# Kernel tuning notes

Measured on AMD Instinct MI355X. Metric: run time of the kernel, lower is better.

The kernel has to match this reference:

```python
import jax, jax.numpy as jnp
import numpy as np

K = 3  # kernel size, padding=1, stride=1


def _patches(x):
    # x: [N,C,H,W] -> [N,C,9,H,W] of 3x3 neighborhoods (zero pad 1)
    N, C, H, W = x.shape
    xp = jnp.pad(x, ((0, 0), (0, 0), (1, 1), (1, 1)))
    return jnp.stack([xp[:, :, i:i + H, j:j + W] for i in range(K) for j in range(K)], axis=2)


def _conv25d(x, depth, fx, w0, w1, w2, b):
    # depth-banded 2.5D conv: 3 weight sets selected per (pixel, kernel-tap) by depth band
    N, C, H, W = x.shape
    O = w0.shape[0]
    px = _patches(x)                       # [N,C,9,H,W]
    d = _patches(depth)[:, 0]              # [N,9,H,W]
    center = d[:, K * K // 2:K * K // 2 + 1]  # [N,1,H,W]
    valid = ((d != 0) & (center != 0)).astype(x.dtype)
    d = d * valid
    center = d[:, K * K // 2:K * K // 2 + 1]
    gr = center / fx                       # grid_range, pixel_size = 1
    half = gr * 0.5
    m0 = (jnp.abs(d - (center + gr)) <= half).astype(x.dtype)  # behind plane
    m1 = (jnp.abs(d - center) < half).astype(x.dtype)          # on plane
    m2 = (jnp.abs(d - (center - gr)) <= half).astype(x.dtype)  # in front
    out = jnp.zeros((N, O, H, W), x.dtype)
    for w, m in ((w0, m0), (w1, m1), (w2, m2)):
        out = out + jnp.einsum('ock,nckhw->nohw', w.reshape(O, C, K * K), px * m[:, None])
    return out + b[None, :, None, None]


def _maxpool2(x):
    return jax.lax.reduce_window(x, -jnp.inf, jax.lax.max, (1, 1, 2, 2), (1, 1, 2, 2), 'VALID')


def setup_inputs() -> dict:
    key = jax.random.key(0)
    ks = jax.random.split(key, 16)
    N, H, W = 16, 224, 224

    def xavier(k, shape):
        if len(shape) == 4:
            rf = shape[2] * shape[3]
            fan_in, fan_out = shape[1] * rf, shape[0] * rf
        else:
            fan_out, fan_in = shape
        lim = float(np.sqrt(6.0 / (fan_in + fan_out)))
        return jax.random.uniform(k, shape, jnp.float32, -lim, lim)

    return {
        'x': jax.random.normal(ks[0], (N, 3, H, W), jnp.float32),
        'depth': jax.random.uniform(ks[1], (N, 1, H, W), jnp.float32, 1.0, 5.0),
        'fx': jnp.full((1,), 4.0, jnp.float32),
        'c1_w0': xavier(ks[2], (16, 3, 3, 3)),
        'c1_w1': xavier(ks[3], (16, 3, 3, 3)),
        'c1_w2': xavier(ks[4], (16, 3, 3, 3)),
        'c1_b': jnp.zeros((16,), jnp.float32),
        'c2_w0': xavier(ks[5], (16, 16, 3, 3)),
        'c2_w1': xavier(ks[6], (16, 16, 3, 3)),
        'c2_w2': xavier(ks[7], (16, 16, 3, 3)),
        'c2_b': jnp.zeros((16,), jnp.float32),
        'fc1_w': xavier(ks[8], (128, 16 * (W // 2) * (H // 2))),
        'fc1_b': jnp.zeros((128,), jnp.float32),
        'fc2_w': xavier(ks[9], (10, 128)),
        'fc2_b': jnp.zeros((10,), jnp.float32),
    }


def reference(x, depth, fx, c1_w0, c1_w1, c1_w2, c1_b, c2_w0, c2_w1, c2_w2, c2_b, fc1_w, fc1_b, fc2_w, fc2_b):
    h = jax.nn.relu(_conv25d(x, depth, fx, c1_w0, c1_w1, c1_w2, c1_b))
    h = _maxpool2(jax.nn.relu(_conv25d(h, depth, fx, c2_w0, c2_w1, c2_w2, c2_b)))
    h = h.reshape(h.shape[0], -1)          # [N, 16*112*112]
    h = h @ fc1_w.T + fc1_b                # no relu between fc1/fc2 (matches source)
    h = h @ fc2_w.T + fc2_b
    return jax.nn.log_softmax(h, axis=1)
```

## Files before the change

kernel.cpp:

```cpp
#include <hip/hip_runtime.h>
#include <hip/hip_fp16.h>
#include <stdint.h>

#define HH 224
#define HWD 224
#define HWP (HH*HWD)
#define PH 112
#define PW 112
#define PHW (PH*PW)
#define FCK 200704
#define KSEG 196

typedef _Float16 f16x8 __attribute__((ext_vector_type(8)));
typedef float f32x4 __attribute__((ext_vector_type(4)));

static __device__ __forceinline__ uint32_t pkh2(float a, float b) {
  __half2 h = __floats2half2_rn(a, b);
  return __builtin_bit_cast(uint32_t, h);
}
static __device__ __forceinline__ f32x4 mfma16(uint4 a, uint4 b, f32x4 c) {
  return __builtin_amdgcn_mfma_f32_16x16x32_f16(
      __builtin_bit_cast(f16x8, a), __builtin_bit_cast(f16x8, b), c, 0, 0, 0);
}


__global__ __launch_bounds__(256, 4) void conv1_kernel(
    const float* __restrict__ x, const float* __restrict__ depth,
    const float* __restrict__ fxp,
    const float* __restrict__ w0, const float* __restrict__ w1,
    const float* __restrict__ w2, const float* __restrict__ bias,
    uint32_t* __restrict__ sel, __half* __restrict__ h1t) {
  __shared__ __align__(16) __half ts[324*24];
  __shared__ __align__(16) uint4 wlds[15*64];
  __shared__ float dt[324];
  __shared__ uint32_t sbits[256];
  __shared__ __align__(16) __half hbuf[1024];
  int tid = threadIdx.x;
  int lane = tid & 63, wid = tid >> 6;
  int r = lane & 15;
  int tapPar = lane >> 5;
  int c0 = ((lane >> 4) & 1) * 8;
  float bo = bias[r];
  float fx = fxp[0];

  #pragma unroll
  for (int it = 0; it < 4; ++it) {
    int t = tid + it*256;
    int tc = min(t, 959);
    int ln = tc & 63; int pj = tc >> 6;
    int p = pj / 3, j = pj % 3;
    int o = ln & 15; int tap = p*2 + (ln >> 5);
    int cbase = ((ln >> 4) & 1) * 8;
    const float* wj = (j == 0) ? w0 : (j == 1) ? w1 : w2;
    float f[8];
    #pragma unroll
    for (int e = 0; e < 8; ++e) {
      int c = cbase + e;
      float v = wj[o*27 + min(c,2)*9 + min(tap,8)];
      f[e] = (tap <= 8 && c < 3) ? v : 0.f;
    }
    if (t < 960) {
      uint4 wv = { pkh2(f[0],f[1]), pkh2(f[2],f[3]), pkh2(f[4],f[5]), pkh2(f[6],f[7]) };
      wlds[pj*64 + ln] = wv;
    }
  }

  int tbase = blockIdx.x * 4;
  float pf[2][3]; float pd[2];
  {
    int tile = tbase;
    int n = tile/196, rem = tile%196, br = rem/14, bc = rem%14;
    int y0 = br*16 - 1, x0 = bc*16 - 1;
    const float* xn = x + (size_t)n*3*HWP;
    const float* dn = depth + (size_t)n*HWP;
    #pragma unroll
    for (int it = 0; it < 2; ++it) {
      int p = min(tid + it*256, 323);
      int yy = y0 + p/18, xx = x0 + p%18;
      int gy = min(max(yy,0),HH-1), gx = min(max(xx,0),HWD-1);
      size_t off = (size_t)gy*HWD + gx;
      pf[it][0] = xn[off]; pf[it][1] = xn[HWP+off]; pf[it][2] = xn[2*HWP+off];
      float dv = dn[off];
      pd[it] = (yy>=0 && yy<HH && xx>=0 && xx<HWD) ? dv : 0.f;
    }
  }

  for (int ti = 0; ti < 4; ++ti) {
    int tile = tbase + ti;
    int n = tile/196, rem = tile%196, br = rem/14, bc = rem%14;
    #pragma unroll
    for (int it = 0; it < 2; ++it) {
      int p = tid + it*256;
      if (p < 324) {
        uint4 v0 = { pkh2(pf[it][0], pf[it][1]), pkh2(pf[it][2], 0.f), 0u, 0u };
        uint4 z  = { 0u, 0u, 0u, 0u };
        *(uint4*)(ts + p*24)      = v0;
        *(uint4*)(ts + p*24 + 8)  = z;
        *(uint4*)(ts + p*24 + 16) = z;
        dt[p] = pd[it];
      }
    }
    if (ti < 3) {
      int tile2 = tile + 1;
      int n2 = tile2/196, rem2 = tile2%196, br2 = rem2/14, bc2 = rem2%14;
      int y0 = br2*16 - 1, x0 = bc2*16 - 1;
      const float* xn = x + (size_t)n2*3*HWP;
      const float* dn = depth + (size_t)n2*HWP;
      #pragma unroll
      for (int it = 0; it < 2; ++it) {
        int p = min(tid + it*256, 323);
        int yy = y0 + p/18, xx = x0 + p%18;
        int gy = min(max(yy,0),HH-1), gx = min(max(xx,0),HWD-1);
        size_t off = (size_t)gy*HWD + gx;
        pf[it][0] = xn[off]; pf[it][1] = xn[HWP+off]; pf[it][2] = xn[2*HWP+off];
        float dv = dn[off];
        pd[it] = (yy>=0 && yy<HH && xx>=0 && xx<HWD) ? dv : 0.f;
      }
    }
    __syncthreads();
    {
      int py = tid >> 4, px = tid & 15;
      float c = dt[(py+1)*18 + (px+1)];
      float gr = c / fx;
      float hf = gr * 0.5f;
      uint32_t bits = 0;
      #pragma unroll
      for (int i = 0; i < 3; ++i)
        #pragma unroll
        for (int j = 0; j < 3; ++j) {
          float d = dt[(py+i)*18 + (px+j)];
          int k = i*3 + j;
          uint32_t bb = 0;
          if (fabsf(d - (c + gr)) <= hf) bb |= 1u;
          if (fabsf(d - c) < hf)         bb |= 2u;
          if (fabsf(d - (c - gr)) <= hf) bb |= 4u;
          bits |= bb << (3*k);
        }
      sbits[tid] = bits;
      sel[(size_t)n*HWP + (br*16 + py)*HWD + bc*16 + px] = bits;
    }
    __syncthreads();
    uint32_t svc[4];
    #pragma unroll
    for (int ty = 0; ty < 4; ++ty) svc[ty] = sbits[(wid*4 + ty)*16 + r];
    f32x4 acc[4] = {{0,0,0,0},{0,0,0,0},{0,0,0,0},{0,0,0,0}};
    #pragma unroll
    for (int p = 0; p < 5; ++p) {
      int ta = 2*p, tb = (2*p+1 > 8) ? 8 : 2*p+1;
      int dyL = tapPar ? tb/3 : ta/3;
      int dxL = tapPar ? tb%3 : ta%3;
      int shL = 3*(tapPar ? 2*p+1 : 2*p);
      uint4 a[4];
      #pragma unroll
      for (int ty = 0; ty < 4; ++ty) {
        int ly = wid*4 + ty;
        a[ty] = *(const uint4*)(ts + ((ly + dyL)*18 + (r + dxL))*24 + c0);
      }
      #pragma unroll
      for (int j = 0; j < 3; ++j) {
        uint4 bf = wlds[(p*3 + j)*64 + lane];
        #pragma unroll
        for (int ty = 0; ty < 4; ++ty) {
          uint32_t msk = 0u - ((svc[ty] >> (shL + j)) & 1u);
          uint4 am = { a[ty].x & msk, a[ty].y & msk, a[ty].z & msk, a[ty].w & msk };
          acc[ty] = mfma16(am, bf, acc[ty]);
        }
      }
    }
    #pragma unroll
    for (int ty = 0; ty < 4; ++ty) {
      int gy = br*16 + wid*4 + ty;
      #pragma unroll
      for (int e = 0; e < 4; ++e) {
        float v = fmaxf(acc[ty][e] + bo, 0.f);
        hbuf[wid*256 + ((lane>>4)*4 + e)*16 + r] = __float2half(v);
      }
      uint2 hw = *(uint2*)&hbuf[wid*256 + lane*4];
      *(uint2*)(h1t + ((size_t)(n*HWP + gy*HWD) + bc*16)*16 + lane*4) = hw;
    }
    __syncthreads();
  }
}

__global__ __launch_bounds__(256, 4) void conv2_kernel(
    const __half* __restrict__ h1t, const uint32_t* __restrict__ sel,
    const float* __restrict__ w0, const float* __restrict__ w1,
    const float* __restrict__ w2, const float* __restrict__ bias,
    __half* __restrict__ pooled) {
  __shared__ __align__(16) __half ts[324*24];
  __shared__ __align__(16) uint4 wlds[15*64];
  __shared__ float pl[64*17];
  int tid = threadIdx.x;
  int lane = tid & 63, wid = tid >> 6;
  int r = lane & 15;
  int tapPar = lane >> 5;
  int c0 = ((lane >> 4) & 1) * 8;
  float bo = bias[r];

  #pragma unroll
  for (int it = 0; it < 4; ++it) {
    int t = tid + it*256;
    int tc = min(t, 959);
    int ln = tc & 63; int pj = tc >> 6;
    int p = pj / 3, j = pj % 3;
    int o = ln & 15; int tap = p*2 + (ln >> 5);
    int cbase = ((ln >> 4) & 1) * 8;
    const float* wj = (j == 0) ? w0 : (j == 1) ? w1 : w2;
    const float* wp = wj + o*144 + cbase*9 + tap;
    float f[8];
    #pragma unroll
    for (int e = 0; e < 8; ++e) {
      float v = wp[e*9];
      f[e] = (tap <= 8) ? v : 0.f;
    }
    if (t < 960) {
      uint4 wv = { pkh2(f[0],f[1]), pkh2(f[2],f[3]), pkh2(f[4],f[5]), pkh2(f[6],f[7]) };
      wlds[pj*64 + ln] = wv;
    }
  }

  int tbase = blockIdx.x * 4;
  uint4 st[3]; uint32_t sv[4];
  {
    int tile = tbase;
    int n = tile/196, rem = tile%196, br = rem/14, bc = rem%14;
    int y0 = br*16 - 1, x0 = bc*16 - 1;
    const __half* hn = h1t + (size_t)n*HWP*16;
    #pragma unroll
    for (int it = 0; it < 3; ++it) {
      int w = min(tid + it*256, 647);
      int p = w >> 1, hh = w & 1;
      int gy = min(max(y0 + p/18, 0), HH-1);
      int gx = min(max(x0 + p%18, 0), HWD-1);
      st[it] = *(const uint4*)(hn + ((size_t)(gy*HWD + gx))*16 + hh*8);
    }
    #pragma unroll
    for (int ty = 0; ty < 4; ++ty)
      sv[ty] = sel[(size_t)n*HWP + (br*16 + wid*4 + ty)*HWD + bc*16 + r];
  }

  for (int ti = 0; ti < 4; ++ti) {
    int tile = tbase + ti;
    int n = tile/196, rem = tile%196, br = rem/14, bc = rem%14;
    #pragma unroll
    for (int it = 0; it < 3; ++it) {
      int w = tid + it*256;
      if (w < 648) {
        int p = w >> 1, hh = w & 1;
        *(uint4*)(ts + p*24 + hh*8) = st[it];
      }
    }
    uint32_t svc[4];
    #pragma unroll
    for (int ty = 0; ty < 4; ++ty) svc[ty] = sv[ty];
    if (ti < 3) {
      int tile2 = tile + 1;
      int n2 = tile2/196, rem2 = tile2%196, br2 = rem2/14, bc2 = rem2%14;
      int y0 = br2*16 - 1, x0 = bc2*16 - 1;
      const __half* hn = h1t + (size_t)n2*HWP*16;
      #pragma unroll
      for (int it = 0; it < 3; ++it) {
        int w = min(tid + it*256, 647);
        int p = w >> 1, hh = w & 1;
        int gy = min(max(y0 + p/18, 0), HH-1);
        int gx = min(max(x0 + p%18, 0), HWD-1);
        st[it] = *(const uint4*)(hn + ((size_t)(gy*HWD + gx))*16 + hh*8);
      }
      #pragma unroll
      for (int ty = 0; ty < 4; ++ty)
        sv[ty] = sel[(size_t)n2*HWP + (br2*16 + wid*4 + ty)*HWD + bc2*16 + r];
    }
    __syncthreads();
    f32x4 acc[4] = {{0,0,0,0},{0,0,0,0},{0,0,0,0},{0,0,0,0}};
    #pragma unroll
    for (int p = 0; p < 5; ++p) {
      int ta = 2*p, tb = (2*p+1 > 8) ? 8 : 2*p+1;
      int dyL = tapPar ? tb/3 : ta/3;
      int dxL = tapPar ? tb%3 : ta%3;
      int shL = 3*(tapPar ? 2*p+1 : 2*p);
      uint4 a[4];
      #pragma unroll
      for (int ty = 0; ty < 4; ++ty) {
        int ly = wid*4 + ty;
        a[ty] = *(const uint4*)(ts + ((ly + dyL)*18 + (r + dxL))*24 + c0);
      }
      #pragma unroll
      for (int j = 0; j < 3; ++j) {
        uint4 bf = wlds[(p*3 + j)*64 + lane];
        #pragma unroll
        for (int ty = 0; ty < 4; ++ty) {
          uint32_t msk = 0u - ((svc[ty] >> (shL + j)) & 1u);
          uint4 am = { a[ty].x & msk, a[ty].y & msk, a[ty].z & msk, a[ty].w & msk };
          acc[ty] = mfma16(am, bf, acc[ty]);
        }
      }
    }
    #pragma unroll
    for (int yp = 0; yp < 2; ++yp) {
      f32x4 v0 = acc[yp*2], v1 = acc[yp*2+1];
      float m00 = fmaxf(fmaxf(v0[0]+bo, 0.f), fmaxf(v0[1]+bo, 0.f));
      float m01 = fmaxf(fmaxf(v0[2]+bo, 0.f), fmaxf(v0[3]+bo, 0.f));
      float m10 = fmaxf(fmaxf(v1[0]+bo, 0.f), fmaxf(v1[1]+bo, 0.f));
      float m11 = fmaxf(fmaxf(v1[2]+bo, 0.f), fmaxf(v1[3]+bo, 0.f));
      int prow = wid*2 + yp;
      int pc0 = (lane >> 4)*2;
      pl[(prow*8 + pc0)*17 + r]     = fmaxf(m00, m10);
      pl[(prow*8 + pc0 + 1)*17 + r] = fmaxf(m01, m11);
    }
    __syncthreads();
    for (int t = tid; t < 1024; t += 256) {
      int oo = t >> 6; int pix = t & 63;
      int pr = pix >> 3, pc = pix & 7;
      pooled[(size_t)(n*16 + oo)*PHW + (br*8 + pr)*PW + bc*8 + pc] =
          __float2half(pl[pix*17 + oo]);
    }
    __syncthreads();
  }
}

__global__ __launch_bounds__(256) void fc1_kernel(
    const __half* __restrict__ hin, const float* __restrict__ wgt,
    float* __restrict__ partial) {
  __shared__ __align__(16) uint4 alds[2][256];
  __shared__ __align__(16) uint4 wlds[2][2][256];
  __shared__ __align__(16) f32x4 cacc[2][256];
  int tid = threadIdx.x;
  int grp  = blockIdx.x / 196;
  int kseg = blockIdx.x % 196;
  int obase = grp * 32;
  int lane = tid & 63, wid = tid >> 6;
  int q8 = tid & 15, row = tid >> 4;
  int sslot = (q8>>2)*64 + (row | ((q8&3) << 4));
  const __half* hp0 = hin + (size_t)row*FCK + kseg*1024 + q8*8;
  const float* wq0  = wgt + (size_t)(obase + row)*FCK + kseg*1024 + q8*8;
  const float* wq1  = wgt + (size_t)(obase + 16 + row)*FCK + kseg*1024 + q8*8;
  uint4 hv; float4 w0a, w0b, w1a, w1b;
  hv  = *(const uint4*)hp0;
  w0a = *(const float4*)wq0; w0b = *(const float4*)(wq0 + 4);
  w1a = *(const float4*)wq1; w1b = *(const float4*)(wq1 + 4);
  f32x4 acc0 = {0,0,0,0}, acc1 = {0,0,0,0};
  for (int ch = 0; ch < 8; ++ch) {
    int buf = ch & 1;
    alds[buf][sslot] = hv;
    wlds[buf][0][sslot] = (uint4){ pkh2(w0a.x,w0a.y), pkh2(w0a.z,w0a.w),
                                   pkh2(w0b.x,w0b.y), pkh2(w0b.z,w0b.w) };
    wlds[buf][1][sslot] = (uint4){ pkh2(w1a.x,w1a.y), pkh2(w1a.z,w1a.w),
                                   pkh2(w1b.x,w1b.y), pkh2(w1b.z,w1b.w) };
    if (ch < 7) {
      hv  = *(const uint4*)(hp0 + (ch+1)*128);
      w0a = *(const float4*)(wq0 + (ch+1)*128); w0b = *(const float4*)(wq0 + (ch+1)*128 + 4);
      w1a = *(const float4*)(wq1 + (ch+1)*128); w1b = *(const float4*)(wq1 + (ch+1)*128 + 4);
    }
    __syncthreads();
    uint4 av = alds[buf][wid*64 + lane];
    acc0 = mfma16(av, wlds[buf][0][wid*64 + lane], acc0);
    acc1 = mfma16(av, wlds[buf][1][wid*64 + lane], acc1);
  }
  cacc[0][wid*64 + lane] = acc0;
  cacc[1][wid*64 + lane] = acc1;
  __syncthreads();
  {
    int l = tid & 63, e = tid >> 6;
    int nn = (l >> 4)*4 + e;
    int oo = l & 15;
    #pragma unroll
    for (int g = 0; g < 2; ++g) {
      float s = cacc[g][l][e] + cacc[g][64 + l][e] + cacc[g][128 + l][e] + cacc[g][192 + l][e];
      partial[((size_t)kseg*16 + nn)*128 + obase + g*16 + oo] = s;
    }
  }
}

__global__ __launch_bounds__(128) void fc2_kernel(
    const float* __restrict__ partial, const float* __restrict__ fc1b,
    const float* __restrict__ w, const float* __restrict__ b,
    float* __restrict__ out) {
  __shared__ float row[128];
  __shared__ float v[10];
  __shared__ float lse;
  int n = blockIdx.x, t = threadIdx.x;
  float s = fc1b[t];
  for (int k = 0; k < KSEG; ++k) s += partial[((size_t)k*16 + n)*128 + t];
  row[t] = s;
  __syncthreads();
  if (t < 10) {
    float sv = b[t];
    const float* wr = w + t*128;
    for (int i = 0; i < 128; ++i) sv += row[i]*wr[i];
    v[t] = sv;
  }
  __syncthreads();
  if (t == 0) {
    float m = v[0];
    for (int i = 1; i < 10; ++i) m = fmaxf(m, v[i]);
    float se = 0.f;
    for (int i = 0; i < 10; ++i) se += expf(v[i] - m);
    lse = m + logf(se);
  }
  __syncthreads();
  if (t < 10) out[n*10 + t] = v[t] - lse;
}

extern "C" void kernel_launch(void* const* d_in, const int* in_sizes, int n_in,
                              void* d_out, int out_size, void* d_ws, size_t ws_size,
                              hipStream_t stream) {
  const float* x     = (const float*)d_in[0];
  const float* depth = (const float*)d_in[1];
  const float* fx    = (const float*)d_in[2];
  const float* c1w0  = (const float*)d_in[3];
  const float* c1w1  = (const float*)d_in[4];
  const float* c1w2  = (const float*)d_in[5];
  const float* c1b   = (const float*)d_in[6];
  const float* c2w0  = (const float*)d_in[7];
  const float* c2w1  = (const float*)d_in[8];
  const float* c2w2  = (const float*)d_in[9];
  const float* c2b   = (const float*)d_in[10];
  const float* fc1w  = (const float*)d_in[11];
  const float* fc1b  = (const float*)d_in[12];
  const float* fc2w  = (const float*)d_in[13];
  const float* fc2b  = (const float*)d_in[14];
  float* out = (float*)d_out;

  char* ws = (char*)d_ws;
  uint32_t* sel  = (uint32_t*)ws;
  __half* h1t    = (__half*)(ws + 3211264);
  __half* pooled = (__half*)(ws + 28901376);
  float* partial = (float*)(ws + 35323904);

  conv1_kernel<<<784, 256, 0, stream>>>(x, depth, fx, c1w0, c1w1, c1w2, c1b, sel, h1t);
  conv2_kernel<<<784, 256, 0, stream>>>(h1t, sel, c2w0, c2w1, c2w2, c2b, pooled);
  fc1_kernel<<<784, 256, 0, stream>>>(pooled, fc1w, partial);
  fc2_kernel<<<16, 128, 0, stream>>>(partial, fc1b, fc2w, fc2b, out);
}
```

Before: 104.8 us.

## Double-buffer conv tiles, add nontemporal loads, remap fc1 blocks, parallelize fc2

The conv1 and conv2 shared-memory tile buffers are now double-buffered, which lets the trailing per-tile barrier be removed, and occupancy hints drop from 4 to 3 blocks. Streaming global loads of inputs, h1t, sel and the fc1 weights become nontemporal loads. The fc1 block-to-(kseg, group) mapping is permuted so concurrently running blocks are spread across segments. fc2 now uses 256 threads with a two-way split of the partial reduction and wave-shuffle dot products. Together these aim to cut barrier stalls, cache pollution and serial tail work, at the cost of more LDS per block and lower occupancy.

```diff
diff --git a/kernel.cpp b/kernel.cpp
--- a/kernel.cpp
+++ b/kernel.cpp
@@ -13,6 +13,8 @@
 
 typedef _Float16 f16x8 __attribute__((ext_vector_type(8)));
 typedef float f32x4 __attribute__((ext_vector_type(4)));
+typedef float f32x4v __attribute__((ext_vector_type(4)));
+typedef uint32_t u32x4v __attribute__((ext_vector_type(4)));
 
 static __device__ __forceinline__ uint32_t pkh2(float a, float b) {
   __half2 h = __floats2half2_rn(a, b);
@@ -22,17 +24,25 @@
   return __builtin_amdgcn_mfma_f32_16x16x32_f16(
       __builtin_bit_cast(f16x8, a), __builtin_bit_cast(f16x8, b), c, 0, 0, 0);
 }
-
-
-__global__ __launch_bounds__(256, 4) void conv1_kernel(
+static __device__ __forceinline__ uint4 ntld_u4(const void* p) {
+  u32x4v v = __builtin_nontemporal_load((const u32x4v*)p);
+  return (uint4){v.x, v.y, v.z, v.w};
+}
+static __device__ __forceinline__ float4 ntld_f4(const void* p) {
+  f32x4v v = __builtin_nontemporal_load((const f32x4v*)p);
+  return make_float4(v.x, v.y, v.z, v.w);
+}
+
+
+__global__ __launch_bounds__(256, 3) void conv1_kernel(
     const float* __restrict__ x, const float* __restrict__ depth,
     const float* __restrict__ fxp,
     const float* __restrict__ w0, const float* __restrict__ w1,
     const float* __restrict__ w2, const float* __restrict__ bias,
     uint32_t* __restrict__ sel, __half* __restrict__ h1t) {
-  __shared__ __align__(16) __half ts[324*24];
+  __shared__ __align__(16) __half ts[2][324*24];
   __shared__ __align__(16) uint4 wlds[15*64];
-  __shared__ float dt[324];
+  __shared__ float dt[2][324];
   __shared__ uint32_t sbits[256];
   __shared__ __align__(16) __half hbuf[1024];
   int tid = threadIdx.x;
@@ -79,13 +89,16 @@
       int yy = y0 + p/18, xx = x0 + p%18;
       int gy = min(max(yy,0),HH-1), gx = min(max(xx,0),HWD-1);
       size_t off = (size_t)gy*HWD + gx;
-      pf[it][0] = xn[off]; pf[it][1] = xn[HWP+off]; pf[it][2] = xn[2*HWP+off];
-      float dv = dn[off];
+      pf[it][0] = __builtin_nontemporal_load(xn + off);
+      pf[it][1] = __builtin_nontemporal_load(xn + HWP + off);
+      pf[it][2] = __builtin_nontemporal_load(xn + 2*HWP + off);
+      float dv = __builtin_nontemporal_load(dn + off);
       pd[it] = (yy>=0 && yy<HH && xx>=0 && xx<HWD) ? dv : 0.f;
     }
   }
 
   for (int ti = 0; ti < 4; ++ti) {
+    int cur = ti & 1;
     int tile = tbase + ti;
     int n = tile/196, rem = tile%196, br = rem/14, bc = rem%14;
     #pragma unroll
@@ -94,10 +107,10 @@
       if (p < 324) {
         uint4 v0 = { pkh2(pf[it][0], pf[it][1]), pkh2(pf[it][2], 0.f), 0u, 0u };
         uint4 z  = { 0u, 0u, 0u, 0u };
-        *(uint4*)(ts + p*24)      = v0;
-        *(uint4*)(ts + p*24 + 8)  = z;
-        *(uint4*)(ts + p*24 + 16) = z;
-        dt[p] = pd[it];
+        *(uint4*)(&ts[cur][0] + p*24)      = v0;
+        *(uint4*)(&ts[cur][0] + p*24 + 8)  = z;
+        *(uint4*)(&ts[cur][0] + p*24 + 16) = z;
+        dt[cur][p] = pd[it];
       }
     }
     if (ti < 3) {
@@ -112,15 +125,17 @@
         int yy = y0 + p/18, xx = x0 + p%18;
         int gy = min(max(yy,0),HH-1), gx = min(max(xx,0),HWD-1);
         size_t off = (size_t)gy*HWD + gx;
-        pf[it][0] = xn[off]; pf[it][1] = xn[HWP+off]; pf[it][2] = xn[2*HWP+off];
-        float dv = dn[off];
+        pf[it][0] = __builtin_nontemporal_load(xn + off);
+        pf[it][1] = __builtin_nontemporal_load(xn + HWP + off);
+        pf[it][2] = __builtin_nontemporal_load(xn + 2*HWP + off);
+        float dv = __builtin_nontemporal_load(dn + off);
         pd[it] = (yy>=0 && yy<HH && xx>=0 && xx<HWD) ? dv : 0.f;
       }
     }
     __syncthreads();
     {
       int py = tid >> 4, px = tid & 15;
-      float c = dt[(py+1)*18 + (px+1)];
+      float c = dt[cur][(py+1)*18 + (px+1)];
       float gr = c / fx;
       float hf = gr * 0.5f;
       uint32_t bits = 0;
@@ -128,7 +143,7 @@
       for (int i = 0; i < 3; ++i)
         #pragma unroll
         for (int j = 0; j < 3; ++j) {
-          float d = dt[(py+i)*18 + (px+j)];
+          float d = dt[cur][(py+i)*18 + (px+j)];
           int k = i*3 + j;
           uint32_t bb = 0;
           if (fabsf(d - (c + gr)) <= hf) bb |= 1u;
@@ -154,7 +169,7 @@
       #pragma unroll
       for (int ty = 0; ty < 4; ++ty) {
         int ly = wid*4 + ty;
-        a[ty] = *(const uint4*)(ts + ((ly + dyL)*18 + (r + dxL))*24 + c0);
+        a[ty] = *(const uint4*)(&ts[cur][0] + ((ly + dyL)*18 + (r + dxL))*24 + c0);
       }
       #pragma unroll
       for (int j = 0; j < 3; ++j) {
@@ -178,16 +193,15 @@
       uint2 hw = *(uint2*)&hbuf[wid*256 + lane*4];
       *(uint2*)(h1t + ((size_t)(n*HWP + gy*HWD) + bc*16)*16 + lane*4) = hw;
     }
-    __syncthreads();
-  }
-}
-
-__global__ __launch_bounds__(256, 4) void conv2_kernel(
+  }
+}
+
+__global__ __launch_bounds__(256, 3) void conv2_kernel(
     const __half* __restrict__ h1t, const uint32_t* __restrict__ sel,
     const float* __restrict__ w0, const float* __restrict__ w1,
     const float* __restrict__ w2, const float* __restrict__ bias,
     __half* __restrict__ pooled) {
-  __shared__ __align__(16) __half ts[324*24];
+  __shared__ __align__(16) __half ts[2][324*24];
   __shared__ __align__(16) uint4 wlds[15*64];
   __shared__ float pl[64*17];
   int tid = threadIdx.x;
@@ -232,14 +246,16 @@
       int p = w >> 1, hh = w & 1;
       int gy = min(max(y0 + p/18, 0), HH-1);
       int gx = min(max(x0 + p%18, 0), HWD-1);
-      st[it] = *(const uint4*)(hn + ((size_t)(gy*HWD + gx))*16 + hh*8);
+      st[it] = ntld_u4(hn + ((size_t)(gy*HWD + gx))*16 + hh*8);
     }
     #pragma unroll
     for (int ty = 0; ty < 4; ++ty)
-      sv[ty] = sel[(size_t)n*HWP + (br*16 + wid*4 + ty)*HWD + bc*16 + r];
+      sv[ty] = __builtin_nontemporal_load(
+          sel + (size_t)n*HWP + (br*16 + wid*4 + ty)*HWD + bc*16 + r);
   }
 
   for (int ti = 0; ti < 4; ++ti) {
+    int cur = ti & 1;
     int tile = tbase + ti;
     int n = tile/196, rem = tile%196, br = rem/14, bc = rem%14;
     #pragma unroll
@@ -247,7 +263,7 @@
       int w = tid + it*256;
       if (w < 648) {
         int p = w >> 1, hh = w & 1;
-        *(uint4*)(ts + p*24 + hh*8) = st[it];
+        *(uint4*)(&ts[cur][0] + p*24 + hh*8) = st[it];
       }
     }
     uint32_t svc[4];
@@ -264,11 +280,12 @@
         int p = w >> 1, hh = w & 1;
         int gy = min(max(y0 + p/18, 0), HH-1);
         int gx = min(max(x0 + p%18, 0), HWD-1);
-        st[it] = *(const uint4*)(hn + ((size_t)(gy*HWD + gx))*16 + hh*8);
+        st[it] = ntld_u4(hn + ((size_t)(gy*HWD + gx))*16 + hh*8);
       }
       #pragma unroll
       for (int ty = 0; ty < 4; ++ty)
-        sv[ty] = sel[(size_t)n2*HWP + (br2*16 + wid*4 + ty)*HWD + bc2*16 + r];
+        sv[ty] = __builtin_nontemporal_load(
+            sel + (size_t)n2*HWP + (br2*16 + wid*4 + ty)*HWD + bc2*16 + r);
     }
     __syncthreads();
     f32x4 acc[4] = {{0,0,0,0},{0,0,0,0},{0,0,0,0},{0,0,0,0}};
@@ -282,7 +299,7 @@
       #pragma unroll
       for (int ty = 0; ty < 4; ++ty) {
         int ly = wid*4 + ty;
-        a[ty] = *(const uint4*)(ts + ((ly + dyL)*18 + (r + dxL))*24 + c0);
+        a[ty] = *(const uint4*)(&ts[cur][0] + ((ly + dyL)*18 + (r + dxL))*24 + c0);
       }
       #pragma unroll
       for (int j = 0; j < 3; ++j) {
@@ -314,7 +331,6 @@
       pooled[(size_t)(n*16 + oo)*PHW + (br*8 + pr)*PW + bc*8 + pc] =
           __float2half(pl[pix*17 + oo]);
     }
-    __syncthreads();
   }
 }
 
@@ -325,8 +341,10 @@
   __shared__ __align__(16) uint4 wlds[2][2][256];
   __shared__ __align__(16) f32x4 cacc[2][256];
   int tid = threadIdx.x;
-  int grp  = blockIdx.x / 196;
-  int kseg = blockIdx.x % 196;
+  int b = blockIdx.x;
+  int snum = (b & 7)*98 + (b >> 3);
+  int kseg = snum >> 2;
+  int grp  = snum & 3;
   int obase = grp * 32;
   int lane = tid & 63, wid = tid >> 6;
   int q8 = tid & 15, row = tid >> 4;
@@ -336,8 +354,8 @@
   const float* wq1  = wgt + (size_t)(obase + 16 + row)*FCK + kseg*1024 + q8*8;
   uint4 hv; float4 w0a, w0b, w1a, w1b;
   hv  = *(const uint4*)hp0;
-  w0a = *(const float4*)wq0; w0b = *(const float4*)(wq0 + 4);
-  w1a = *(const float4*)wq1; w1b = *(const float4*)(wq1 + 4);
+  w0a = ntld_f4(wq0); w0b = ntld_f4(wq0 + 4);
+  w1a = ntld_f4(wq1); w1b = ntld_f4(wq1 + 4);
   f32x4 acc0 = {0,0,0,0}, acc1 = {0,0,0,0};
   for (int ch = 0; ch < 8; ++ch) {
     int buf = ch & 1;
@@ -348,8 +366,8 @@
                                    pkh2(w1b.x,w1b.y), pkh2(w1b.z,w1b.w) };
     if (ch < 7) {
       hv  = *(const uint4*)(hp0 + (ch+1)*128);
-      w0a = *(const float4*)(wq0 + (ch+1)*128); w0b = *(const float4*)(wq0 + (ch+1)*128 + 4);
-      w1a = *(const float4*)(wq1 + (ch+1)*128); w1b = *(const float4*)(wq1 + (ch+1)*128 + 4);
+      w0a = ntld_f4(wq0 + (ch+1)*128); w0b = ntld_f4(wq0 + (ch+1)*128 + 4);
+      w1a = ntld_f4(wq1 + (ch+1)*128); w1b = ntld_f4(wq1 + (ch+1)*128 + 4);
     }
     __syncthreads();
     uint4 av = alds[buf][wid*64 + lane];
@@ -371,23 +389,35 @@
   }
 }
 
-__global__ __launch_bounds__(128) void fc2_kernel(
+__global__ __launch_bounds__(256) void fc2_kernel(
     const float* __restrict__ partial, const float* __restrict__ fc1b,
     const float* __restrict__ w, const float* __restrict__ b,
     float* __restrict__ out) {
+  __shared__ float psum[256];
   __shared__ float row[128];
   __shared__ float v[10];
   __shared__ float lse;
   int n = blockIdx.x, t = threadIdx.x;
-  float s = fc1b[t];
-  for (int k = 0; k < KSEG; ++k) s += partial[((size_t)k*16 + n)*128 + t];
-  row[t] = s;
+  {
+    int o = t & 127, half = t >> 7;
+    const float* pp = partial + ((size_t)(half*98)*16 + n)*128 + o;
+    float s = 0.f;
+    for (int k = 0; k < 98; ++k)
+      s += __builtin_nontemporal_load(pp + (size_t)k*2048);
+    psum[t] = s;
+  }
   __syncthreads();
-  if (t < 10) {
-    float sv = b[t];
-    const float* wr = w + t*128;
-    for (int i = 0; i < 128; ++i) sv += row[i]*wr[i];
-    v[t] = sv;
+  if (t < 128) row[t] = fc1b[t] + psum[t] + psum[t + 128];
+  __syncthreads();
+  {
+    int wv = t >> 6, lane = t & 63;
+    for (int d = wv; d < 10; d += 4) {
+      float acc = w[d*128 + lane]*row[lane] + w[d*128 + 64 + lane]*row[64 + lane];
+      acc += __shfl_xor(acc, 1);  acc += __shfl_xor(acc, 2);
+      acc += __shfl_xor(acc, 4);  acc += __shfl_xor(acc, 8);
+      acc += __shfl_xor(acc, 16); acc += __shfl_xor(acc, 32);
+      if (lane == 0) v[d] = acc + b[d];
+    }
   }
   __syncthreads();
   if (t == 0) {
@@ -430,5 +460,5 @@
   conv1_kernel<<<784, 256, 0, stream>>>(x, depth, fx, c1w0, c1w1, c1w2, c1b, sel, h1t);
   conv2_kernel<<<784, 256, 0, stream>>>(h1t, sel, c2w0, c2w1, c2w2, c2b, pooled);
   fc1_kernel<<<784, 256, 0, stream>>>(pooled, fc1w, partial);
-  fc2_kernel<<<16, 128, 0, stream>>>(partial, fc1b, fc2w, fc2b, out);
-}
+  fc2_kernel<<<16, 256, 0, stream>>>(partial, fc1b, fc2w, fc2b, out);
+}
```

New measurement: 113.2 us. 8.1% more time.
